# Optimization experiments

Hardware: AMD Instinct MI355X
Metric: run time of the kernel (lower is better)

## Reference

```python
import jax, jax.numpy as jnp
import numpy as np

B, N, F = 8, 512, 128
H, U = 4, 32
LEAKY_ALPHA = 0.2

def setup_inputs() -> dict:
    key = jax.random.key(0)
    k1, k2, k3, k4 = jax.random.split(key, 4)
    inputs = jax.random.normal(k1, (B, N, F), dtype=jnp.float32)
    # glorot-ish scaled params
    W_src = jax.random.normal(k2, (H, F, U), dtype=jnp.float32) * (2.0 / (F + U)) ** 0.5
    W_dst = jax.random.normal(k3, (H, F, U), dtype=jnp.float32) * (2.0 / (F + U)) ** 0.5
    a = jax.random.normal(k4, (H, U, 1), dtype=jnp.float32) * (2.0 / (U + 1)) ** 0.5
    return {"inputs": inputs, "W_src": W_src, "W_dst": W_dst, "a": a}

def reference(inputs, W_src, W_dst, a):
    # GATv2, eval mode (no dropout). Loop over the small fixed head count to
    # keep peak memory at one (B,N,N,U) pairwise tensor at a time, matching
    # the original per-head loop.
    outs = []
    for h in range(W_src.shape[0]):
        h_src = inputs @ W_src[h]          # (B, N, U)
        h_dst = inputs @ W_dst[h]          # (B, N, U)
        # pairwise[b,i,j,:] = h_src[b,i] + h_dst[b,j]
        pair = jax.nn.leaky_relu(h_src[:, :, None, :] + h_dst[:, None, :, :],
                                 negative_slope=LEAKY_ALPHA)  # (B,N,N,U)
        scores = jnp.einsum('biju,u->bij', pair, a[h, :, 0])   # (B,N,N)
        attn = jax.nn.softmax(scores, axis=-1)
        outs.append(attn @ h_src)          # (B,N,U) -- weighted sum of h_src
    return jnp.concatenate(outs, axis=-1)  # concat_heads=True -> (B,N,H*U)
```

## Files before the change

kernel.cpp:

```cpp
#include <hip/hip_runtime.h>
#include <hip/hip_bf16.h>

#define B_ 8
#define N_ 512
#define F_ 128
#define H_ 4
#define U_ 32
#define LEAKY_ALPHA 0.2f
#define PS 520

typedef __attribute__((ext_vector_type(8))) short short8;
typedef __attribute__((ext_vector_type(4))) float f32x4;

static __device__ __forceinline__ short f2bf_s(float x) {
    __hip_bfloat16 hv = __float2bfloat16(x);
    return *reinterpret_cast<short*>(&hv);
}
static __device__ __forceinline__ float bf2f_s(short v) {
    return __uint_as_float(((unsigned)(unsigned short)v) << 16);
}

__global__ __launch_bounds__(256) void proj_kernel(
    const float* __restrict__ x, const float* __restrict__ Wsrc,
    const float* __restrict__ Wdst, const float* __restrict__ a,
    float* __restrict__ hsrc, float* __restrict__ hdstNT,
    float* __restrict__ Drow, float* __restrict__ ascaled,
    short* __restrict__ hsrcT)
{
    __shared__ float4 xlds[8 * 32];
    const int t  = threadIdx.x;
    const int r0 = blockIdx.x * 8;

    const float4* xg = (const float4*)x + (size_t)r0 * 32;
    xlds[t] = xg[t];
    __syncthreads();

    const int u     = t & 31;
    const int h     = (t >> 5) & 3;
    const int which = t >> 7;
    const float* W  = (which ? Wdst : Wsrc) + h * (F_ * U_) + u;

    float acc[8];
#pragma unroll
    for (int r = 0; r < 8; ++r) acc[r] = 0.f;

#pragma unroll 2
    for (int fc = 0; fc < 32; ++fc) {
        const float w0 = W[(4 * fc + 0) * U_];
        const float w1 = W[(4 * fc + 1) * U_];
        const float w2 = W[(4 * fc + 2) * U_];
        const float w3 = W[(4 * fc + 3) * U_];
#pragma unroll
        for (int r = 0; r < 8; ++r) {
            const float4 xv = xlds[r * 32 + fc];
            float s = acc[r];
            s = fmaf(xv.x, w0, s);
            s = fmaf(xv.y, w1, s);
            s = fmaf(xv.z, w2, s);
            s = fmaf(xv.w, w3, s);
            acc[r] = s;
        }
    }

    const float av = a[h * U_ + u];
    if (which == 1 && blockIdx.x == 0)
        ascaled[h * U_ + u] = (1.f - LEAKY_ALPHA) * av;

    const int b  = r0 >> 9;
    const int n0 = r0 & (N_ - 1);
    const int bh = b * H_ + h;

    if (which == 0) {
        short8 pk;
#pragma unroll
        for (int r = 0; r < 8; ++r) {
            const size_t base = ((size_t)(bh * N_ + n0 + r) << 5) + u;
            hsrc[base] = acc[r];
            pk[r] = f2bf_s(acc[r]);
        }
        *(short8*)&hsrcT[((size_t)(bh * U_) + u) * N_ + n0] = pk;
    } else {
        float4 v0, v1;
        v0.x = -acc[0]; v0.y = -acc[1]; v0.z = -acc[2]; v0.w = -acc[3];
        v1.x = -acc[4]; v1.y = -acc[5]; v1.z = -acc[6]; v1.w = -acc[7];
        float* dst = hdstNT + ((size_t)(bh * U_) + u) * N_ + n0;
        *(float4*)dst       = v0;
        *(float4*)(dst + 4) = v1;
#pragma unroll
        for (int r = 0; r < 8; ++r) {
            float v = acc[r] * av;
            v += __shfl_xor(v, 1);
            v += __shfl_xor(v, 2);
            v += __shfl_xor(v, 4);
            v += __shfl_xor(v, 8);
            v += __shfl_xor(v, 16);
            if (u == 0) Drow[bh * N_ + n0 + r] = v;
        }
    }
}

__global__ __launch_bounds__(512, 4) void attn_kernel(
    const float* __restrict__ hsrc, const float* __restrict__ hdstNT,
    const float* __restrict__ Drow, const float* __restrict__ ascaled,
    const short* __restrict__ hsrcT, float* __restrict__ out)
{
    __shared__ __align__(16) short pbf[16 * PS];
    __shared__ f32x4 scr[8][64];
    __shared__ float lfin[16];

    const int t    = threadIdx.x;
    const int L    = t & 63;
    const int w    = __builtin_amdgcn_readfirstlane(t >> 6);
    const int tile = blockIdx.x & 31;
    const int bh   = blockIdx.x >> 5;
    const int h    = bh & 3;
    const int b    = bh >> 2;
    const size_t bhN = (size_t)bh * N_;
    const int ig0  = tile * 16;
    const int j    = t;

    const float* dT = hdstNT + ((size_t)bh * U_) * N_ + j;
#define DL(k) float d##k = dT[(k) * N_];
    DL(0) DL(1) DL(2) DL(3) DL(4) DL(5) DL(6) DL(7)
    DL(8) DL(9) DL(10) DL(11) DL(12) DL(13) DL(14) DL(15)
    DL(16) DL(17) DL(18) DL(19) DL(20) DL(21) DL(22) DL(23)
    DL(24) DL(25) DL(26) DL(27) DL(28) DL(29) DL(30) DL(31)
#undef DL
#define PIN4(a0,a1,a2,a3) asm volatile("" : "+v"(a0), "+v"(a1), "+v"(a2), "+v"(a3));
    PIN4(d0,d1,d2,d3)     PIN4(d4,d5,d6,d7)
    PIN4(d8,d9,d10,d11)   PIN4(d12,d13,d14,d15)
    PIN4(d16,d17,d18,d19) PIN4(d20,d21,d22,d23)
    PIN4(d24,d25,d26,d27) PIN4(d28,d29,d30,d31)
#undef PIN4

    const float Dj = Drow[bhN + j];
    const float* sB = hsrc + ((bhN + ig0) << 5);
    const float* aS = ascaled + h * U_;

#define TERM(k, dk, accv) accv = fmaf(aS[k], fmaxf(sR[k], dk), accv);
#pragma unroll 2
    for (int i = 0; i < 16; ++i) {
        const float* sR = sB + (i << 5);
        float acA = 0.f, acB = 0.f;
        TERM(0,  d0,  acA) TERM(1,  d1,  acB) TERM(2,  d2,  acA) TERM(3,  d3,  acB)
        TERM(4,  d4,  acA) TERM(5,  d5,  acB) TERM(6,  d6,  acA) TERM(7,  d7,  acB)
        TERM(8,  d8,  acA) TERM(9,  d9,  acB) TERM(10, d10, acA) TERM(11, d11, acB)
        TERM(12, d12, acA) TERM(13, d13, acB) TERM(14, d14, acA) TERM(15, d15, acB)
        TERM(16, d16, acA) TERM(17, d17, acB) TERM(18, d18, acA) TERM(19, d19, acB)
        TERM(20, d20, acA) TERM(21, d21, acB) TERM(22, d22, acA) TERM(23, d23, acB)
        TERM(24, d24, acA) TERM(25, d25, acB) TERM(26, d26, acA) TERM(27, d27, acB)
        TERM(28, d28, acA) TERM(29, d29, acB) TERM(30, d30, acA) TERM(31, d31, acB)
        const float e = __expf(Dj + acA + acB);
        pbf[i * PS + j] = f2bf_s(e);
    }
#undef TERM
    __syncthreads();

    {
        const int ri = t >> 5;
        const int rg = t & 31;
        const short8* pr = (const short8*)(pbf + ri * PS + rg * 16);
        const short8 pa = pr[0];
        const short8 pb = pr[1];
        float sum = 0.f;
#pragma unroll
        for (int k = 0; k < 8; ++k) sum += bf2f_s(pa[k]) + bf2f_s(pb[k]);
        sum += __shfl_xor(sum, 1);
        sum += __shfl_xor(sum, 2);
        sum += __shfl_xor(sum, 4);
        sum += __shfl_xor(sum, 8);
        sum += __shfl_xor(sum, 16);
        if (rg == 0) lfin[ri] = __builtin_amdgcn_rcpf(sum);
    }

    const int m  = L & 15;
    const int kq = L >> 4;
    const int nt = w & 1;
    const int ks = w >> 1;
    const short* Ap = pbf + m * PS + ks * 128 + kq * 8;
    const short* Bp = hsrcT + ((size_t)bh * U_ + nt * 16 + m) * N_ + ks * 128 + kq * 8;

    f32x4 acc = {0.f, 0.f, 0.f, 0.f};
#pragma unroll
    for (int st = 0; st < 4; ++st) {
        const short8 af = *(const short8*)(Ap + st * 32);
        const short8 bf = *(const short8*)(Bp + st * 32);
        acc = __builtin_amdgcn_mfma_f32_16x16x32_bf16(af, bf, acc, 0, 0, 0);
    }
    scr[w][L] = acc;
    __syncthreads();

    if (w < 2) {
        f32x4 s0 = scr[w][L];
        const f32x4 s1 = scr[w + 2][L];
        const f32x4 s2 = scr[w + 4][L];
        const f32x4 s3 = scr[w + 6][L];
        s0 += s1; s0 += s2; s0 += s3;
#pragma unroll
        for (int r = 0; r < 4; ++r) {
            const int il = kq * 4 + r;
            out[((size_t)(b * N_ + ig0 + il)) * (H_ * U_) + h * U_ + w * 16 + m]
                = s0[r] * lfin[il];
        }
    }
}

extern "C" void kernel_launch(void* const* d_in, const int* in_sizes, int n_in,
                              void* d_out, int out_size, void* d_ws, size_t ws_size,
                              hipStream_t stream) {
    const float* x    = (const float*)d_in[0];
    const float* Wsrc = (const float*)d_in[1];
    const float* Wdst = (const float*)d_in[2];
    const float* a    = (const float*)d_in[3];

    float* ws      = (float*)d_ws;
    float* hsrc    = ws;
    float* hdstNT  = hsrc + (size_t)B_ * H_ * N_ * U_;
    float* Drow    = hdstNT + (size_t)B_ * H_ * U_ * N_;
    float* ascaled = Drow + (size_t)B_ * H_ * N_;
    short* hsrcT   = (short*)(ascaled + H_ * U_);

    proj_kernel<<<(B_ * N_) / 8, 256, 0, stream>>>(x, Wsrc, Wdst, a,
                                                   hsrc, hdstNT, Drow, ascaled,
                                                   hsrcT);
    attn_kernel<<<B_ * H_ * (N_ / 16), 512, 0, stream>>>(hsrc, hdstNT, Drow,
                                                         ascaled, hsrcT,
                                                         (float*)d_out);
}
```

Before: 98.12 us.

## Compute src and dst projections per thread and prefetch hsrc rows in attention

New measurement: 99.05 us. Within noise of the previous version (+1.0%).

```diff
diff --git a/kernel.cpp b/kernel.cpp
--- a/kernel.cpp
+++ b/kernel.cpp
@@ -10,6 +10,7 @@
 #define PS 520
 
 typedef __attribute__((ext_vector_type(8))) short short8;
+typedef __attribute__((ext_vector_type(4))) short short4v;
 typedef __attribute__((ext_vector_type(4))) float f32x4;
 
 static __device__ __forceinline__ short f2bf_s(float x) {
@@ -20,82 +21,81 @@
     return __uint_as_float(((unsigned)(unsigned short)v) << 16);
 }
 
-__global__ __launch_bounds__(256) void proj_kernel(
+__global__ __launch_bounds__(512) void proj_kernel(
     const float* __restrict__ x, const float* __restrict__ Wsrc,
     const float* __restrict__ Wdst, const float* __restrict__ a,
     float* __restrict__ hsrc, float* __restrict__ hdstNT,
     float* __restrict__ Drow, float* __restrict__ ascaled,
     short* __restrict__ hsrcT)
 {
-    __shared__ float4 xlds[8 * 32];
+    __shared__ float4 xlds[16 * 32];
     const int t  = threadIdx.x;
-    const int r0 = blockIdx.x * 8;
-
-    const float4* xg = (const float4*)x + (size_t)r0 * 32;
-    xlds[t] = xg[t];
+    const int r0 = blockIdx.x * 16;
+
+    xlds[t] = ((const float4*)x)[(size_t)r0 * 32 + t];
     __syncthreads();
 
-    const int u     = t & 31;
-    const int h     = (t >> 5) & 3;
-    const int which = t >> 7;
-    const float* W  = (which ? Wdst : Wsrc) + h * (F_ * U_) + u;
-
-    float acc[8];
-#pragma unroll
-    for (int r = 0; r < 8; ++r) acc[r] = 0.f;
+    const int u  = t & 31;
+    const int h  = (t >> 5) & 3;
+    const int rq = t >> 7;
+    const float* Ws = Wsrc + h * (F_ * U_) + u;
+    const float* Wd = Wdst + h * (F_ * U_) + u;
+
+    float as[4], ad[4];
+#pragma unroll
+    for (int r = 0; r < 4; ++r) { as[r] = 0.f; ad[r] = 0.f; }
 
 #pragma unroll 2
     for (int fc = 0; fc < 32; ++fc) {
-        const float w0 = W[(4 * fc + 0) * U_];
-        const float w1 = W[(4 * fc + 1) * U_];
-        const float w2 = W[(4 * fc + 2) * U_];
-        const float w3 = W[(4 * fc + 3) * U_];
-#pragma unroll
-        for (int r = 0; r < 8; ++r) {
-            const float4 xv = xlds[r * 32 + fc];
-            float s = acc[r];
-            s = fmaf(xv.x, w0, s);
-            s = fmaf(xv.y, w1, s);
-            s = fmaf(xv.z, w2, s);
-            s = fmaf(xv.w, w3, s);
-            acc[r] = s;
+        const float s0 = Ws[(4 * fc + 0) * U_];
+        const float s1 = Ws[(4 * fc + 1) * U_];
+        const float s2 = Ws[(4 * fc + 2) * U_];
+        const float s3 = Ws[(4 * fc + 3) * U_];
+        const float d0 = Wd[(4 * fc + 0) * U_];
+        const float d1 = Wd[(4 * fc + 1) * U_];
+        const float d2 = Wd[(4 * fc + 2) * U_];
+        const float d3 = Wd[(4 * fc + 3) * U_];
+#pragma unroll
+        for (int r = 0; r < 4; ++r) {
+            const float4 xv = xlds[(rq * 4 + r) * 32 + fc];
+            float vs = as[r], vd = ad[r];
+            vs = fmaf(xv.x, s0, vs);  vd = fmaf(xv.x, d0, vd);
+            vs = fmaf(xv.y, s1, vs);  vd = fmaf(xv.y, d1, vd);
+            vs = fmaf(xv.z, s2, vs);  vd = fmaf(xv.z, d2, vd);
+            vs = fmaf(xv.w, s3, vs);  vd = fmaf(xv.w, d3, vd);
+            as[r] = vs; ad[r] = vd;
         }
     }
 
     const float av = a[h * U_ + u];
-    if (which == 1 && blockIdx.x == 0)
+    if (t < 128 && blockIdx.x == 0)
         ascaled[h * U_ + u] = (1.f - LEAKY_ALPHA) * av;
 
     const int b  = r0 >> 9;
-    const int n0 = r0 & (N_ - 1);
+    const int n0 = (r0 & (N_ - 1)) + rq * 4;
     const int bh = b * H_ + h;
 
-    if (which == 0) {
-        short8 pk;
-#pragma unroll
-        for (int r = 0; r < 8; ++r) {
-            const size_t base = ((size_t)(bh * N_ + n0 + r) << 5) + u;
-            hsrc[base] = acc[r];
-            pk[r] = f2bf_s(acc[r]);
-        }
-        *(short8*)&hsrcT[((size_t)(bh * U_) + u) * N_ + n0] = pk;
-    } else {
-        float4 v0, v1;
-        v0.x = -acc[0]; v0.y = -acc[1]; v0.z = -acc[2]; v0.w = -acc[3];
-        v1.x = -acc[4]; v1.y = -acc[5]; v1.z = -acc[6]; v1.w = -acc[7];
-        float* dst = hdstNT + ((size_t)(bh * U_) + u) * N_ + n0;
-        *(float4*)dst       = v0;
-        *(float4*)(dst + 4) = v1;
-#pragma unroll
-        for (int r = 0; r < 8; ++r) {
-            float v = acc[r] * av;
-            v += __shfl_xor(v, 1);
-            v += __shfl_xor(v, 2);
-            v += __shfl_xor(v, 4);
-            v += __shfl_xor(v, 8);
-            v += __shfl_xor(v, 16);
-            if (u == 0) Drow[bh * N_ + n0 + r] = v;
-        }
+    short4v pk;
+#pragma unroll
+    for (int r = 0; r < 4; ++r) {
+        hsrc[((size_t)(bh * N_ + n0 + r) << 5) + u] = as[r];
+        pk[r] = f2bf_s(as[r]);
+    }
+    *(short4v*)&hsrcT[((size_t)(bh * U_) + u) * N_ + n0] = pk;
+
+    float4 nv;
+    nv.x = -ad[0]; nv.y = -ad[1]; nv.z = -ad[2]; nv.w = -ad[3];
+    *(float4*)&hdstNT[((size_t)(bh * U_) + u) * N_ + n0] = nv;
+
+#pragma unroll
+    for (int r = 0; r < 4; ++r) {
+        float v = ad[r] * av;
+        v += __shfl_xor(v, 1);
+        v += __shfl_xor(v, 2);
+        v += __shfl_xor(v, 4);
+        v += __shfl_xor(v, 8);
+        v += __shfl_xor(v, 16);
+        if (u == 0) Drow[bh * N_ + n0 + r] = v;
     }
 }
 
@@ -118,6 +118,13 @@
     const size_t bhN = (size_t)bh * N_;
     const int ig0  = tile * 16;
     const int j    = t;
+
+    const float* sB = hsrc + ((bhN + ig0) << 5);
+
+    {
+        const float warm = sB[t];
+        asm volatile("" :: "v"(warm));
+    }
 
     const float* dT = hdstNT + ((size_t)bh * U_) * N_ + j;
 #define DL(k) float d##k = dT[(k) * N_];
@@ -134,7 +141,6 @@
 #undef PIN4
 
     const float Dj = Drow[bhN + j];
-    const float* sB = hsrc + ((bhN + ig0) << 5);
     const float* aS = ascaled + h * U_;
 
 #define TERM(k, dk, accv) accv = fmaf(aS[k], fmaxf(sR[k], dk), accv);
@@ -220,9 +226,9 @@
     float* ascaled = Drow + (size_t)B_ * H_ * N_;
     short* hsrcT   = (short*)(ascaled + H_ * U_);
 
-    proj_kernel<<<(B_ * N_) / 8, 256, 0, stream>>>(x, Wsrc, Wdst, a,
-                                                   hsrc, hdstNT, Drow, ascaled,
-                                                   hsrcT);
+    proj_kernel<<<(B_ * N_) / 16, 512, 0, stream>>>(x, Wsrc, Wdst, a,
+                                                    hsrc, hdstNT, Drow, ascaled,
+                                                    hsrcT);
     attn_kernel<<<B_ * H_ * (N_ / 16), 512, 0, stream>>>(hsrc, hdstNT, Drow,
                                                          ascaled, hsrcT,
                                                          (float*)d_out);
```
